# Optimization experiments

Measured on AMD Instinct MI355X. Metric: run time of the kernel, lower is better.

The kernel has to match this reference:

```python
import jax, jax.numpy as jnp
import numpy as np

U = 2000; V = 2000; F = 2000; R = 5; H = 64; O = 75; SH = 64; SF = 128


def setup_inputs() -> dict:
    key = jax.random.key(0)
    ks = jax.random.split(key, 16)
    inp = {
        'feature_u': jax.random.uniform(ks[0], (U, F), jnp.float32),
        'feature_v': jax.random.uniform(ks[1], (V, F), jnp.float32),
        'M_u': jax.random.uniform(ks[2], (R, U, V), jnp.float32) * 0.01,
        'M_v': jax.random.uniform(ks[3], (R, V, U), jnp.float32) * 0.01,
        'W': jax.random.normal(ks[4], (R, F, H), jnp.float32) * 0.02,
        'Q': jax.random.normal(ks[5], (R, O, O), jnp.float32) * 0.1,
        'side_feature_u': jax.random.normal(ks[6], (U, SF), jnp.float32),
        'side_feature_v': jax.random.normal(ks[7], (V, SF), jnp.float32),
        'w_side_u': jax.random.normal(ks[8], (SF, SH), jnp.float32) * 0.05,
        'b_side_u': jnp.zeros((SH,), jnp.float32),
        'g_side_u': jnp.ones((SH,), jnp.float32),
        'beta_side_u': jnp.zeros((SH,), jnp.float32),
        'w_side_v': jax.random.normal(ks[9], (SF, SH), jnp.float32) * 0.05,
        'b_side_v': jnp.zeros((SH,), jnp.float32),
        'g_side_v': jnp.ones((SH,), jnp.float32),
        'beta_side_v': jnp.zeros((SH,), jnp.float32),
        'w_cat_u': jax.random.normal(ks[10], (2 * R * H + SH, O), jnp.float32) * 0.05,
        'b_cat_u': jnp.zeros((O,), jnp.float32),
        'g_cat_u': jnp.ones((O,), jnp.float32),
        'beta_cat_u': jnp.zeros((O,), jnp.float32),
        'w_cat_v': jax.random.normal(ks[11], (2 * R * H + SH, O), jnp.float32) * 0.05,
        'b_cat_v': jnp.zeros((O,), jnp.float32),
        'g_cat_v': jnp.ones((O,), jnp.float32),
        'beta_cat_v': jnp.zeros((O,), jnp.float32),
    }
    return inp


def _bn_relu(x, g, b, eps=1e-5):
    # BatchNorm1d in training mode (biased batch variance) followed by ReLU
    mu = x.mean(0)
    var = jnp.mean((x - mu) ** 2, axis=0)
    return jax.nn.relu((x - mu) * jax.lax.rsqrt(var + eps) * g + b)


def reference(feature_u, feature_v, M_u, M_v, W, Q,
              side_feature_u, side_feature_v,
              w_side_u, b_side_u, g_side_u, beta_side_u,
              w_side_v, b_side_v, g_side_v, beta_side_v,
              w_cat_u, b_cat_u, g_cat_u, beta_cat_u,
              w_cat_v, b_cat_v, g_cat_v, beta_cat_v):
    # drop_out = 0.0 -> sparse_drop is identity
    # per-relation message passing: hidden_u[r] = relu(M_u[r] @ (feature_v @ W[r]))
    hv_pre = jnp.einsum('vf,rfh->rvh', feature_v, W)           # [R,V,H]
    hidden_u = jax.nn.relu(jnp.einsum('ruv,rvh->ruh', M_u, hv_pre))  # [R,U,H]
    hu_pre = jnp.einsum('uf,rfh->ruh', feature_u, W)           # [R,U,H]
    hidden_v = jax.nn.relu(jnp.einsum('rvu,ruh->rvh', M_v, hu_pre))  # [R,V,H]
    # concat over relations along feature dim (matches torch.cat(list, dim=1))
    hu_cat = jnp.transpose(hidden_u, (1, 0, 2)).reshape(hidden_u.shape[1], -1)  # [U, R*H]
    hv_cat = jnp.transpose(hidden_v, (1, 0, 2)).reshape(hidden_v.shape[1], -1)  # [V, R*H]
    W_flat = jnp.transpose(W, (1, 0, 2)).reshape(W.shape[1], -1)                # [F, R*H]
    cat_u = jnp.concatenate([hu_cat, feature_u @ W_flat], axis=1)  # [U, 2*R*H]
    cat_v = jnp.concatenate([hv_cat, feature_v @ W_flat], axis=1)
    # side feature branches: Linear -> BatchNorm -> ReLU
    side_u = _bn_relu(side_feature_u @ w_side_u + b_side_u, g_side_u, beta_side_u)
    side_v = _bn_relu(side_feature_v @ w_side_v + b_side_v, g_side_v, beta_side_v)
    cat_u = jnp.concatenate([cat_u, side_u], axis=1)
    cat_v = jnp.concatenate([cat_v, side_v], axis=1)
    embed_u = _bn_relu(cat_u @ w_cat_u + b_cat_u, g_cat_u, beta_cat_u)  # [U,O]
    embed_v = _bn_relu(cat_v @ w_cat_v + b_cat_v, g_cat_v, beta_cat_v)  # [V,O]
    # per-relation bilinear score: embed_u @ Q[r] @ embed_v.T, stacked -> [R,U,V]
    score = jnp.einsum('uo,rop,vp->ruv', embed_u, Q, embed_v)
    return score
```

## Files before the change

kernel.cpp:

```cpp
#include <hip/hip_runtime.h>

#define U_DIM 2000
#define V_DIM 2000
#define F_DIM 2000
#define R_DIM 5
#define H_DIM 64
#define O_DIM 75
#define SH_DIM 64
#define SF_DIM 128
#define CAT_DIM (2 * R_DIM * H_DIM + SH_DIM)

struct G2 {
  const float* A0; const float* B0; float* C0;
  const float* A1; const float* B1; float* C1;
  long sA0, sB0, sC0, sA1, sB1, sC1;
  int zSplit, M, N, K;
};

template<bool KSPLIT>
__launch_bounds__(256)
__global__ void gemm64(G2 g) {
  const int z = blockIdx.z;
  const float *A, *B;
  float* C;
  if (z < g.zSplit) {
    A = g.A0 + (long)z * g.sA0; B = g.B0 + (long)z * g.sB0; C = g.C0 + (long)z * g.sC0;
  } else {
    const int zi = z - g.zSplit;
    A = g.A1 + (long)zi * g.sA1; B = g.B1 + (long)zi * g.sB1; C = g.C1 + (long)zi * g.sC1;
  }
  const int M = g.M, N = g.N, K = g.K;
  const int row0 = blockIdx.x << 6;
  int col0, kbeg, kend;
  if (KSPLIT) {
    col0 = 0;
    const int kch = (K + (int)gridDim.y - 1) / (int)gridDim.y;
    kbeg = (int)blockIdx.y * kch;
    kend = min(K, kbeg + kch);
    C += (long)blockIdx.y * (long)gridDim.z * (long)M * N;
  } else {
    col0 = (int)blockIdx.y << 6;
    kbeg = 0; kend = K;
  }

  __shared__ float As[16][68];
  __shared__ float Bs[16][64];

  const int tid = threadIdx.x;
  const int ar = tid >> 2, ak4 = (tid & 3) << 2;
  const int bk = tid >> 4, bn4 = (tid & 15) << 2;
  const int tx = tid & 15, ty = tid >> 4;

  const bool arow_ok = (row0 + ar) < M;
  const long Arow = (long)(row0 + ar) * K;
  const bool avec = ((K & 3) == 0);
  const bool bvec = ((N & 3) == 0);

  float acc[4][4];
#pragma unroll
  for (int i = 0; i < 4; ++i)
#pragma unroll
    for (int j = 0; j < 4; ++j) acc[i][j] = 0.f;

  for (int k0 = kbeg; k0 < kend; k0 += 16) {
    {
      const int gk = k0 + ak4;
      float4 a4;
      if (arow_ok && avec && gk + 3 < kend) {
        a4 = *reinterpret_cast<const float4*>(A + Arow + gk);
      } else {
        a4.x = (arow_ok && gk + 0 < kend) ? A[Arow + gk + 0] : 0.f;
        a4.y = (arow_ok && gk + 1 < kend) ? A[Arow + gk + 1] : 0.f;
        a4.z = (arow_ok && gk + 2 < kend) ? A[Arow + gk + 2] : 0.f;
        a4.w = (arow_ok && gk + 3 < kend) ? A[Arow + gk + 3] : 0.f;
      }
      As[ak4 + 0][ar] = a4.x;
      As[ak4 + 1][ar] = a4.y;
      As[ak4 + 2][ar] = a4.z;
      As[ak4 + 3][ar] = a4.w;
    }
    {
      const int gkb = k0 + bk, gn = col0 + bn4;
      float4 b4;
      if (gkb < kend && bvec && gn + 3 < N) {
        b4 = *reinterpret_cast<const float4*>(B + (long)gkb * N + gn);
      } else {
        const long rb = (long)gkb * N;
        b4.x = (gkb < kend && gn + 0 < N) ? B[rb + gn + 0] : 0.f;
        b4.y = (gkb < kend && gn + 1 < N) ? B[rb + gn + 1] : 0.f;
        b4.z = (gkb < kend && gn + 2 < N) ? B[rb + gn + 2] : 0.f;
        b4.w = (gkb < kend && gn + 3 < N) ? B[rb + gn + 3] : 0.f;
      }
      *reinterpret_cast<float4*>(&Bs[bk][bn4]) = b4;
    }
    __syncthreads();
#pragma unroll
    for (int k = 0; k < 16; ++k) {
      const float4 av = *reinterpret_cast<const float4*>(&As[k][ty << 2]);
      const float4 bv = *reinterpret_cast<const float4*>(&Bs[k][tx << 2]);
      const float aa[4] = {av.x, av.y, av.z, av.w};
      const float bb[4] = {bv.x, bv.y, bv.z, bv.w};
#pragma unroll
      for (int i = 0; i < 4; ++i)
#pragma unroll
        for (int j = 0; j < 4; ++j) acc[i][j] = fmaf(aa[i], bb[j], acc[i][j]);
    }
    __syncthreads();
  }

  const int c0 = col0 + (tx << 2);
#pragma unroll
  for (int i = 0; i < 4; ++i) {
    const int r = row0 + (ty << 2) + i;
    if (r >= M) continue;
    if (bvec && c0 + 3 < N) {
      float4 v;
      v.x = acc[i][0]; v.y = acc[i][1]; v.z = acc[i][2]; v.w = acc[i][3];
      *reinterpret_cast<float4*>(C + (long)r * N + c0) = v;
    } else {
#pragma unroll
      for (int j = 0; j < 4; ++j)
        if (c0 + j < N) C[(long)r * N + c0 + j] = acc[i][j];
    }
  }
}

__global__ void reduceKS(const float* __restrict__ P, float* __restrict__ out,
                         long n4, long stride4, int KS, int relu) {
  const float4* p = reinterpret_cast<const float4*>(P);
  float4* o = reinterpret_cast<float4*>(out);
  for (long i = (long)blockIdx.x * blockDim.x + threadIdx.x; i < n4;
       i += (long)gridDim.x * blockDim.x) {
    float4 s = p[i];
    for (int ks = 1; ks < KS; ++ks) {
      float4 t = p[i + (long)ks * stride4];
      s.x += t.x; s.y += t.y; s.z += t.z; s.w += t.w;
    }
    if (relu) {
      s.x = fmaxf(s.x, 0.f); s.y = fmaxf(s.y, 0.f);
      s.z = fmaxf(s.z, 0.f); s.w = fmaxf(s.w, 0.f);
    }
    o[i] = s;
  }
}

__global__ void colstats2(const float* __restrict__ X0, const float* __restrict__ X1,
                          int rows, int C, float* mv0, float* mv1, float eps) {
  const float* X = blockIdx.y ? X1 : X0;
  float* mv = blockIdx.y ? mv1 : mv0;
  const int c = blockIdx.x;
  float s = 0.f, sq = 0.f;
  for (int r = threadIdx.x; r < rows; r += 256) {
    float x = X[(long)r * C + c];
    s += x;
    sq += x * x;
  }
#pragma unroll
  for (int off = 32; off > 0; off >>= 1) {
    s += __shfl_down(s, off, 64);
    sq += __shfl_down(sq, off, 64);
  }
  __shared__ float sh[2][4];
  const int lane = threadIdx.x & 63, w = threadIdx.x >> 6;
  if (lane == 0) { sh[0][w] = s; sh[1][w] = sq; }
  __syncthreads();
  if (threadIdx.x == 0) {
    float S = sh[0][0] + sh[0][1] + sh[0][2] + sh[0][3];
    float SQ = sh[1][0] + sh[1][1] + sh[1][2] + sh[1][3];
    float mu = S / rows;
    float var = SQ / rows - mu * mu;
    mv[c] = mu;
    mv[C + c] = rsqrtf(var + eps);
  }
}

__global__ void bn_apply2(float* X0, float* X1,
                          const float* __restrict__ mv0, const float* __restrict__ mv1,
                          const float* __restrict__ g0, const float* __restrict__ b0,
                          const float* __restrict__ g1, const float* __restrict__ b1,
                          int rows, int C, float* XT1) {
  const int z = blockIdx.y;
  float* X = z ? X1 : X0;
  const float* mv = z ? mv1 : mv0;
  const float* gg = z ? g1 : g0;
  const float* bb = z ? b1 : b0;
  const long total = (long)rows * C;
  for (long i = (long)blockIdx.x * blockDim.x + threadIdx.x; i < total;
       i += (long)gridDim.x * blockDim.x) {
    int c = (int)(i % C);
    float v = fmaxf((X[i] - mv[c]) * mv[C + c] * gg[c] + bb[c], 0.f);
    X[i] = v;
    if (XT1 && z) {
      int r = (int)(i / C);
      XT1[(long)c * rows + r] = v;
    }
  }
}

__global__ void concat2(const float* __restrict__ hidU, const float* __restrict__ huPre,
                        const float* __restrict__ sideU,
                        const float* __restrict__ hidV, const float* __restrict__ hvPre,
                        const float* __restrict__ sideV,
                        float* catU, float* catV, int rows) {
  const int z = blockIdx.y;
  const float* hid = z ? hidV : hidU;
  const float* pre = z ? hvPre : huPre;
  const float* side = z ? sideV : sideU;
  float* cat = z ? catV : catU;
  const long total = (long)rows * CAT_DIM;
  for (long i = (long)blockIdx.x * blockDim.x + threadIdx.x; i < total;
       i += (long)gridDim.x * blockDim.x) {
    int u = (int)(i / CAT_DIM);
    int j = (int)(i % CAT_DIM);
    float v;
    if (j < R_DIM * H_DIM) {
      v = hid[(long)(j >> 6) * rows * H_DIM + (long)u * H_DIM + (j & 63)];
    } else if (j < 2 * R_DIM * H_DIM) {
      int jj = j - R_DIM * H_DIM;
      v = pre[(long)(jj >> 6) * rows * H_DIM + (long)u * H_DIM + (jj & 63)];
    } else {
      v = side[(long)u * SH_DIM + (j - 2 * R_DIM * H_DIM)];
    }
    cat[i] = v;
  }
}

extern "C" void kernel_launch(void* const* d_in, const int* in_sizes, int n_in,
                              void* d_out, int out_size, void* d_ws, size_t ws_size,
                              hipStream_t stream) {
  (void)in_sizes; (void)n_in; (void)out_size;
  const float* feature_u   = (const float*)d_in[0];
  const float* feature_v   = (const float*)d_in[1];
  const float* M_u         = (const float*)d_in[2];
  const float* M_v         = (const float*)d_in[3];
  const float* W           = (const float*)d_in[4];
  const float* Q           = (const float*)d_in[5];
  const float* side_u_f    = (const float*)d_in[6];
  const float* side_v_f    = (const float*)d_in[7];
  const float* w_side_u    = (const float*)d_in[8];
  const float* g_side_u    = (const float*)d_in[10];
  const float* beta_side_u = (const float*)d_in[11];
  const float* w_side_v    = (const float*)d_in[12];
  const float* g_side_v    = (const float*)d_in[14];
  const float* beta_side_v = (const float*)d_in[15];
  const float* w_cat_u     = (const float*)d_in[16];
  const float* g_cat_u     = (const float*)d_in[18];
  const float* beta_cat_u  = (const float*)d_in[19];
  const float* w_cat_v     = (const float*)d_in[20];
  const float* g_cat_v     = (const float*)d_in[22];
  const float* beta_cat_v  = (const float*)d_in[23];
  float* out = (float*)d_out;

  float* ws = (float*)d_ws;
  long off = 0;
  float* hv_pre   = ws + off; off += (long)R_DIM * V_DIM * H_DIM;
  float* hu_pre   = ws + off; off += (long)R_DIM * U_DIM * H_DIM;
  float* hidden_u = ws + off; off += (long)R_DIM * U_DIM * H_DIM;
  float* hidden_v = ws + off; off += (long)R_DIM * V_DIM * H_DIM;
  float* sideU    = ws + off; off += (long)U_DIM * SH_DIM;
  float* sideV    = ws + off; off += (long)V_DIM * SH_DIM;
  float* catU     = ws + off; off += (long)U_DIM * CAT_DIM;
  float* catV     = ws + off; off += (long)V_DIM * CAT_DIM;
  float* preU     = ws + off; off += (long)U_DIM * O_DIM;
  float* preV     = ws + off; off += (long)V_DIM * O_DIM;
  float* evT      = ws + off; off += (long)O_DIM * V_DIM;
  float* AQ       = ws + off; off += (long)R_DIM * U_DIM * O_DIM;
  float* mvSideU  = ws + off; off += 2 * SH_DIM;
  float* mvSideV  = ws + off; off += 2 * SH_DIM;
  float* mvCatU   = ws + off; off += 2 * O_DIM + 2;
  float* mvCatV   = ws + off; off += 2 * O_DIM + 2;
  float* P        = ws + off;

  const long SLOT = 10L * 2000 * 64;
  const long avail = (long)(ws_size / sizeof(float));
  int KS = 4;
  if (off + 4L * SLOT > avail) KS = 2;
  if (off + (long)KS * SLOT > avail) KS = 1;

  dim3 blk(256);
  const long MN = 2000L * 64;

  {
    G2 g{};
    g.A0 = feature_v; g.B0 = W; g.C0 = P;
    g.sA0 = 0; g.sB0 = (long)F_DIM * H_DIM; g.sC0 = MN;
    g.A1 = feature_u; g.B1 = W; g.C1 = P + 5 * MN;
    g.sA1 = 0; g.sB1 = (long)F_DIM * H_DIM; g.sC1 = MN;
    g.zSplit = R_DIM; g.M = 2000; g.N = H_DIM; g.K = F_DIM;
    gemm64<true><<<dim3(32, KS, 10), blk, 0, stream>>>(g);
  }
  reduceKS<<<1250, blk, 0, stream>>>(P, hv_pre, SLOT / 4, SLOT / 4, KS, 0);

  {
    G2 g{};
    g.A0 = side_u_f; g.B0 = w_side_u; g.C0 = sideU;
    g.sA0 = 0; g.sB0 = 0; g.sC0 = 0;
    g.A1 = side_v_f; g.B1 = w_side_v; g.C1 = sideV;
    g.sA1 = 0; g.sB1 = 0; g.sC1 = 0;
    g.zSplit = 1; g.M = U_DIM; g.N = SH_DIM; g.K = SF_DIM;
    gemm64<false><<<dim3(32, 1, 2), blk, 0, stream>>>(g);
  }

  {
    G2 g{};
    g.A0 = M_u; g.B0 = hv_pre; g.C0 = P;
    g.sA0 = (long)U_DIM * V_DIM; g.sB0 = MN; g.sC0 = MN;
    g.A1 = M_v; g.B1 = hu_pre; g.C1 = P + 5 * MN;
    g.sA1 = (long)V_DIM * U_DIM; g.sB1 = MN; g.sC1 = MN;
    g.zSplit = R_DIM; g.M = 2000; g.N = H_DIM; g.K = 2000;
    gemm64<true><<<dim3(32, KS, 10), blk, 0, stream>>>(g);
  }
  reduceKS<<<1250, blk, 0, stream>>>(P, hidden_u, SLOT / 4, SLOT / 4, KS, 1);

  colstats2<<<dim3(SH_DIM, 2), blk, 0, stream>>>(sideU, sideV, U_DIM, SH_DIM,
                                                 mvSideU, mvSideV, 1e-5f);
  bn_apply2<<<dim3(500, 2), blk, 0, stream>>>(sideU, sideV, mvSideU, mvSideV,
                                              g_side_u, beta_side_u, g_side_v, beta_side_v,
                                              U_DIM, SH_DIM, nullptr);
  concat2<<<dim3(5500, 2), blk, 0, stream>>>(hidden_u, hu_pre, sideU,
                                             hidden_v, hv_pre, sideV, catU, catV, U_DIM);
  {
    G2 g{};
    g.A0 = catU; g.B0 = w_cat_u; g.C0 = preU;
    g.sA0 = 0; g.sB0 = 0; g.sC0 = 0;
    g.A1 = catV; g.B1 = w_cat_v; g.C1 = preV;
    g.sA1 = 0; g.sB1 = 0; g.sC1 = 0;
    g.zSplit = 1; g.M = U_DIM; g.N = O_DIM; g.K = CAT_DIM;
    gemm64<false><<<dim3(32, 2, 2), blk, 0, stream>>>(g);
  }
  colstats2<<<dim3(O_DIM, 2), blk, 0, stream>>>(preU, preV, U_DIM, O_DIM,
                                                mvCatU, mvCatV, 1e-5f);
  bn_apply2<<<dim3(586, 2), blk, 0, stream>>>(preU, preV, mvCatU, mvCatV,
                                              g_cat_u, beta_cat_u, g_cat_v, beta_cat_v,
                                              U_DIM, O_DIM, evT);
  {
    G2 g{};
    g.A0 = preU; g.B0 = Q; g.C0 = AQ;
    g.sA0 = 0; g.sB0 = (long)O_DIM * O_DIM; g.sC0 = (long)U_DIM * O_DIM;
    g.A1 = preU; g.B1 = Q; g.C1 = AQ;
    g.sA1 = 0; g.sB1 = (long)O_DIM * O_DIM; g.sC1 = (long)U_DIM * O_DIM;
    g.zSplit = R_DIM; g.M = U_DIM; g.N = O_DIM; g.K = O_DIM;
    gemm64<false><<<dim3(32, 2, R_DIM), blk, 0, stream>>>(g);
  }
  {
    G2 g{};
    g.A0 = AQ; g.B0 = evT; g.C0 = out;
    g.sA0 = (long)U_DIM * O_DIM; g.sB0 = 0; g.sC0 = (long)U_DIM * V_DIM;
    g.A1 = AQ; g.B1 = evT; g.C1 = out;
    g.sA1 = (long)U_DIM * O_DIM; g.sB1 = 0; g.sC1 = (long)U_DIM * V_DIM;
    g.zSplit = R_DIM; g.M = U_DIM; g.N = V_DIM; g.K = O_DIM;
    gemm64<false><<<dim3(32, 32, R_DIM), blk, 0, stream>>>(g);
  }
}
```

Baseline: 566.4 us.

## Use split-bf16 MFMA GEMM for the large feature, graph and score products

Adds an MFMA-based GEMM kernel that splits each fp32 operand into high and low bf16 parts and accumulates three 16x16x32 bf16 MFMA products, approximating fp32 precision. It replaces the scalar FMA tiled GEMM for the feature projection, the adjacency aggregation and the final score product, and keeps the old kernel for the small GEMMs. The aim is to move the dominant FLOPs onto matrix cores. In exchange it does extra conversion work during tile loading, loads B with scalar non-vectorized reads, and drops the lo*lo term, which slightly reduces accuracy.

Result: faster. 495.3 us (-12.5%).

```diff
diff --git a/kernel.cpp b/kernel.cpp
--- a/kernel.cpp
+++ b/kernel.cpp
@@ -10,6 +10,9 @@
 #define SF_DIM 128
 #define CAT_DIM (2 * R_DIM * H_DIM + SH_DIM)
 
+typedef __attribute__((ext_vector_type(8))) short bf16x8;
+typedef __attribute__((ext_vector_type(4))) float f32x4;
+
 struct G2 {
   const float* A0; const float* B0; float* C0;
   const float* A1; const float* B1; float* C1;
@@ -17,12 +20,20 @@
   int zSplit, M, N, K;
 };
 
+__device__ inline void split2(float x0, float x1, unsigned& h, unsigned& l) {
+  unsigned u0 = __float_as_uint(x0), u1 = __float_as_uint(x1);
+  unsigned h0 = u0 & 0xffff0000u, h1 = u1 & 0xffff0000u;
+  h = (u0 >> 16) | h1;
+  unsigned l0 = __float_as_uint(x0 - __uint_as_float(h0));
+  unsigned l1 = __float_as_uint(x1 - __uint_as_float(h1));
+  l = (l0 >> 16) | (l1 & 0xffff0000u);
+}
+
 template<bool KSPLIT>
 __launch_bounds__(256)
-__global__ void gemm64(G2 g) {
+__global__ void mfma_gemm(G2 g) {
   const int z = blockIdx.z;
-  const float *A, *B;
-  float* C;
+  const float *A, *B; float* C;
   if (z < g.zSplit) {
     A = g.A0 + (long)z * g.sA0; B = g.B0 + (long)z * g.sB0; C = g.C0 + (long)z * g.sC0;
   } else {
@@ -43,6 +54,106 @@
     kbeg = 0; kend = K;
   }
 
+  __shared__ short Ah[4][64][8], Al[4][64][8], Bh[4][64][8], Bl[4][64][8];
+
+  const int tid = threadIdx.x;
+  const int lane = tid & 63;
+  const int w = tid >> 6;
+  const bool kvec = ((K & 3) == 0);
+
+  f32x4 acc[4];
+#pragma unroll
+  for (int c = 0; c < 4; ++c) acc[c] = (f32x4){0.f, 0.f, 0.f, 0.f};
+
+  for (int k0 = kbeg; k0 < kend; k0 += 32) {
+#pragma unroll
+    for (int q = 0; q < 2; ++q) {
+      const int r = (tid >> 3) + (q << 5);
+      const int kq = (tid & 7) << 2;
+      const int gr = row0 + r, gk = k0 + kq;
+      float x0, x1, x2, x3;
+      if (gr < M && kvec && gk + 3 < kend) {
+        const float4 f = *reinterpret_cast<const float4*>(A + (long)gr * K + gk);
+        x0 = f.x; x1 = f.y; x2 = f.z; x3 = f.w;
+      } else {
+        const long rb = (long)gr * K;
+        x0 = (gr < M && gk + 0 < kend) ? A[rb + gk + 0] : 0.f;
+        x1 = (gr < M && gk + 1 < kend) ? A[rb + gk + 1] : 0.f;
+        x2 = (gr < M && gk + 2 < kend) ? A[rb + gk + 2] : 0.f;
+        x3 = (gr < M && gk + 3 < kend) ? A[rb + gk + 3] : 0.f;
+      }
+      unsigned h01, l01, h23, l23;
+      split2(x0, x1, h01, l01);
+      split2(x2, x3, h23, l23);
+      const int t = r >> 4, ln = (r & 15) + (((kq >> 3) & 3) << 4), j0 = kq & 7;
+      uint2 hv; hv.x = h01; hv.y = h23;
+      uint2 lv; lv.x = l01; lv.y = l23;
+      *reinterpret_cast<uint2*>(&Ah[t][ln][j0]) = hv;
+      *reinterpret_cast<uint2*>(&Al[t][ln][j0]) = lv;
+    }
+#pragma unroll
+    for (int q = 0; q < 2; ++q) {
+      const int n = tid & 63;
+      const int kq = ((tid >> 6) + (q << 2)) << 2;
+      const int gn = col0 + n;
+      float xb[4];
+#pragma unroll
+      for (int i2 = 0; i2 < 4; ++i2) {
+        const int gk = k0 + kq + i2;
+        xb[i2] = (gk < kend && gn < N) ? B[(long)gk * N + gn] : 0.f;
+      }
+      unsigned h01, l01, h23, l23;
+      split2(xb[0], xb[1], h01, l01);
+      split2(xb[2], xb[3], h23, l23);
+      const int c = n >> 4, ln = (((kq >> 3) & 3) << 4) + (n & 15), j0 = kq & 7;
+      uint2 hv; hv.x = h01; hv.y = h23;
+      uint2 lv; lv.x = l01; lv.y = l23;
+      *reinterpret_cast<uint2*>(&Bh[c][ln][j0]) = hv;
+      *reinterpret_cast<uint2*>(&Bl[c][ln][j0]) = lv;
+    }
+    __syncthreads();
+    const bf16x8 ah = *reinterpret_cast<const bf16x8*>(&Ah[w][lane][0]);
+    const bf16x8 al = *reinterpret_cast<const bf16x8*>(&Al[w][lane][0]);
+#pragma unroll
+    for (int c = 0; c < 4; ++c) {
+      const bf16x8 bh = *reinterpret_cast<const bf16x8*>(&Bh[c][lane][0]);
+      const bf16x8 bl = *reinterpret_cast<const bf16x8*>(&Bl[c][lane][0]);
+      acc[c] = __builtin_amdgcn_mfma_f32_16x16x32_bf16(ah, bh, acc[c], 0, 0, 0);
+      acc[c] = __builtin_amdgcn_mfma_f32_16x16x32_bf16(ah, bl, acc[c], 0, 0, 0);
+      acc[c] = __builtin_amdgcn_mfma_f32_16x16x32_bf16(al, bh, acc[c], 0, 0, 0);
+    }
+    __syncthreads();
+  }
+
+  const int rbase = (w << 4) + ((lane >> 4) << 2);
+  const int cb = lane & 15;
+#pragma unroll
+  for (int c = 0; c < 4; ++c) {
+    const int col = col0 + (c << 4) + cb;
+    if (col >= N) continue;
+#pragma unroll
+    for (int i = 0; i < 4; ++i) {
+      const int r = row0 + rbase + i;
+      if (r < M) C[(long)r * N + col] = acc[c][i];
+    }
+  }
+}
+
+__launch_bounds__(256)
+__global__ void gemm64(G2 g) {
+  const int z = blockIdx.z;
+  const float *A, *B;
+  float* C;
+  if (z < g.zSplit) {
+    A = g.A0 + (long)z * g.sA0; B = g.B0 + (long)z * g.sB0; C = g.C0 + (long)z * g.sC0;
+  } else {
+    const int zi = z - g.zSplit;
+    A = g.A1 + (long)zi * g.sA1; B = g.B1 + (long)zi * g.sB1; C = g.C1 + (long)zi * g.sC1;
+  }
+  const int M = g.M, N = g.N, K = g.K;
+  const int row0 = blockIdx.x << 6;
+  const int col0 = (int)blockIdx.y << 6;
+
   __shared__ float As[16][68];
   __shared__ float Bs[16][64];
 
@@ -62,17 +173,17 @@
 #pragma unroll
     for (int j = 0; j < 4; ++j) acc[i][j] = 0.f;
 
-  for (int k0 = kbeg; k0 < kend; k0 += 16) {
+  for (int k0 = 0; k0 < K; k0 += 16) {
     {
       const int gk = k0 + ak4;
       float4 a4;
-      if (arow_ok && avec && gk + 3 < kend) {
+      if (arow_ok && avec && gk + 3 < K) {
         a4 = *reinterpret_cast<const float4*>(A + Arow + gk);
       } else {
-        a4.x = (arow_ok && gk + 0 < kend) ? A[Arow + gk + 0] : 0.f;
-        a4.y = (arow_ok && gk + 1 < kend) ? A[Arow + gk + 1] : 0.f;
-        a4.z = (arow_ok && gk + 2 < kend) ? A[Arow + gk + 2] : 0.f;
-        a4.w = (arow_ok && gk + 3 < kend) ? A[Arow + gk + 3] : 0.f;
+        a4.x = (arow_ok && gk + 0 < K) ? A[Arow + gk + 0] : 0.f;
+        a4.y = (arow_ok && gk + 1 < K) ? A[Arow + gk + 1] : 0.f;
+        a4.z = (arow_ok && gk + 2 < K) ? A[Arow + gk + 2] : 0.f;
+        a4.w = (arow_ok && gk + 3 < K) ? A[Arow + gk + 3] : 0.f;
       }
       As[ak4 + 0][ar] = a4.x;
       As[ak4 + 1][ar] = a4.y;
@@ -82,14 +193,14 @@
     {
       const int gkb = k0 + bk, gn = col0 + bn4;
       float4 b4;
-      if (gkb < kend && bvec && gn + 3 < N) {
+      if (gkb < K && bvec && gn + 3 < N) {
         b4 = *reinterpret_cast<const float4*>(B + (long)gkb * N + gn);
       } else {
         const long rb = (long)gkb * N;
-        b4.x = (gkb < kend && gn + 0 < N) ? B[rb + gn + 0] : 0.f;
-        b4.y = (gkb < kend && gn + 1 < N) ? B[rb + gn + 1] : 0.f;
-        b4.z = (gkb < kend && gn + 2 < N) ? B[rb + gn + 2] : 0.f;
-        b4.w = (gkb < kend && gn + 3 < N) ? B[rb + gn + 3] : 0.f;
+        b4.x = (gkb < K && gn + 0 < N) ? B[rb + gn + 0] : 0.f;
+        b4.y = (gkb < K && gn + 1 < N) ? B[rb + gn + 1] : 0.f;
+        b4.z = (gkb < K && gn + 2 < N) ? B[rb + gn + 2] : 0.f;
+        b4.w = (gkb < K && gn + 3 < N) ? B[rb + gn + 3] : 0.f;
       }
       *reinterpret_cast<float4*>(&Bs[bk][bn4]) = b4;
     }
@@ -287,7 +398,7 @@
     g.A1 = feature_u; g.B1 = W; g.C1 = P + 5 * MN;
     g.sA1 = 0; g.sB1 = (long)F_DIM * H_DIM; g.sC1 = MN;
     g.zSplit = R_DIM; g.M = 2000; g.N = H_DIM; g.K = F_DIM;
-    gemm64<true><<<dim3(32, KS, 10), blk, 0, stream>>>(g);
+    mfma_gemm<true><<<dim3(32, KS, 10), blk, 0, stream>>>(g);
   }
   reduceKS<<<1250, blk, 0, stream>>>(P, hv_pre, SLOT / 4, SLOT / 4, KS, 0);
 
@@ -298,7 +409,7 @@
     g.A1 = side_v_f; g.B1 = w_side_v; g.C1 = sideV;
     g.sA1 = 0; g.sB1 = 0; g.sC1 = 0;
     g.zSplit = 1; g.M = U_DIM; g.N = SH_DIM; g.K = SF_DIM;
-    gemm64<false><<<dim3(32, 1, 2), blk, 0, stream>>>(g);
+    gemm64<<<dim3(32, 1, 2), blk, 0, stream>>>(g);
   }
 
   {
@@ -308,7 +419,7 @@
     g.A1 = M_v; g.B1 = hu_pre; g.C1 = P + 5 * MN;
     g.sA1 = (long)V_DIM * U_DIM; g.sB1 = MN; g.sC1 = MN;
     g.zSplit = R_DIM; g.M = 2000; g.N = H_DIM; g.K = 2000;
-    gemm64<true><<<dim3(32, KS, 10), blk, 0, stream>>>(g);
+    mfma_gemm<true><<<dim3(32, KS, 10), blk, 0, stream>>>(g);
   }
   reduceKS<<<1250, blk, 0, stream>>>(P, hidden_u, SLOT / 4, SLOT / 4, KS, 1);
 
@@ -326,7 +437,7 @@
     g.A1 = catV; g.B1 = w_cat_v; g.C1 = preV;
     g.sA1 = 0; g.sB1 = 0; g.sC1 = 0;
     g.zSplit = 1; g.M = U_DIM; g.N = O_DIM; g.K = CAT_DIM;
-    gemm64<false><<<dim3(32, 2, 2), blk, 0, stream>>>(g);
+    gemm64<<<dim3(32, 2, 2), blk, 0, stream>>>(g);
   }
   colstats2<<<dim3(O_DIM, 2), blk, 0, stream>>>(preU, preV, U_DIM, O_DIM,
                                                 mvCatU, mvCatV, 1e-5f);
@@ -340,7 +451,7 @@
     g.A1 = preU; g.B1 = Q; g.C1 = AQ;
     g.sA1 = 0; g.sB1 = (long)O_DIM * O_DIM; g.sC1 = (long)U_DIM * O_DIM;
     g.zSplit = R_DIM; g.M = U_DIM; g.N = O_DIM; g.K = O_DIM;
-    gemm64<false><<<dim3(32, 2, R_DIM), blk, 0, stream>>>(g);
+    gemm64<<<dim3(32, 2, R_DIM), blk, 0, stream>>>(g);
   }
   {
     G2 g{};
@@ -349,6 +460,6 @@
     g.A1 = AQ; g.B1 = evT; g.C1 = out;
     g.sA1 = (long)U_DIM * O_DIM; g.sB1 = 0; g.sC1 = (long)U_DIM * V_DIM;
     g.zSplit = R_DIM; g.M = U_DIM; g.N = V_DIM; g.K = O_DIM;
-    gemm64<false><<<dim3(32, 32, R_DIM), blk, 0, stream>>>(g);
-  }
-}
+    mfma_gemm<false><<<dim3(32, 32, R_DIM), blk, 0, stream>>>(g);
+  }
+}
```
